# Optimization experiments

Hardware: AMD Instinct MI355X
Metric: run time of the kernel (lower is better)

Reference implementation:

```python
import jax, jax.numpy as jnp
import numpy as np

EMBD_DIM = 768
NUM_HEADS = 12
QKV_DIM = EMBD_DIM // NUM_HEADS  # 64


def setup_inputs() -> dict:
    key = jax.random.key(0)
    k1, k2, k3, k4 = jax.random.split(key, 4)
    B, S = 4, 2048
    X = jax.random.normal(k1, (B, S, EMBD_DIM), dtype=jnp.float32)
    mask = jax.random.randint(k2, (B, S), 0, 2, dtype=jnp.int32)
    scale = 1.0 / np.sqrt(EMBD_DIM)
    W_qkv = jax.random.normal(k3, (EMBD_DIM, 3 * EMBD_DIM), dtype=jnp.float32) * scale
    W_fc = jax.random.normal(k4, (EMBD_DIM, EMBD_DIM), dtype=jnp.float32) * scale
    return {"X": X, "mask": mask, "W_qkv": W_qkv, "W_fc": W_fc}


def reference(X, mask, W_qkv, W_fc):
    B, S, _ = X.shape
    qkv = X @ W_qkv  # (B,S,3*E)
    qkv = qkv.reshape(B, S, NUM_HEADS, 3 * QKV_DIM)
    q, k, v = jnp.split(qkv, 3, axis=-1)  # each (B,S,H,d)
    attn = jnp.einsum('bqhd,bkhd->bhqk', q, k) / np.sqrt(QKV_DIM)
    neg_inf = jnp.finfo(attn.dtype).min
    attn = jnp.where(mask[:, None, None, :] == 0, -jnp.inf, attn)
    attn = jax.nn.softmax(attn, axis=-1)
    out = jnp.einsum('bhqv,bvhd->bqhd', attn, v).reshape(B, S, EMBD_DIM)
    return out @ W_fc
```

## Files before the change

kernel.cpp:

```cpp
#include <hip/hip_runtime.h>
#include <hip/hip_bf16.h>
#include <math.h>

#define NB 4
#define NS 2048
#define NE 768
#define NH 12
#define ND 64
#define NQKV 2304
#define BHN (NB*NH)

typedef __attribute__((ext_vector_type(8))) short bf16x8;
typedef __attribute__((ext_vector_type(4))) float f32x4;
typedef __attribute__((ext_vector_type(16))) float f32x16;
typedef unsigned int uint32;

#define QSCALE (0.125f * 1.44269504f)

__device__ __forceinline__ ushort f2bf(float x){
  __hip_bfloat16 h = __float2bfloat16(x);
  return *reinterpret_cast<ushort*>(&h);
}
__device__ __forceinline__ float bf2f(ushort u){
  __hip_bfloat16 h = *reinterpret_cast<__hip_bfloat16*>(&u);
  return __bfloat162float(h);
}
__device__ __forceinline__ void split2(float x, ushort &hi, ushort &lo){
  ushort h = f2bf(x);
  hi = h;
  lo = f2bf(x - bf2f(h));
}
__device__ __forceinline__ uint32 cvtpk(float lo, float hi){
  uint32 r;
  asm("v_cvt_pk_bf16_f32 %0, %1, %2" : "=v"(r) : "v"(lo), "v"(hi));
  return r;
}
__device__ __forceinline__ void pl32swap(uint32 &a, uint32 &b){
  asm("v_permlane32_swap_b32 %0, %1" : "+v"(a), "+v"(b));
}
__device__ __forceinline__ void gl_lds16(const void* g, void* l){
  __builtin_amdgcn_global_load_lds(
      (const __attribute__((address_space(1))) unsigned int*)g,
      (__attribute__((address_space(3))) unsigned int*)l, 16, 0, 0);
}

__global__ __launch_bounds__(256)
void k_convert_x(const float* __restrict__ X, ushort* __restrict__ H, ushort* __restrict__ L)
{
  const int idx = (blockIdx.x*256 + threadIdx.x)*8;
  float4 x0 = *(const float4*)(X+idx);
  float4 x1 = *(const float4*)(X+idx+4);
  float xs[8] = {x0.x,x0.y,x0.z,x0.w,x1.x,x1.y,x1.z,x1.w};
  bf16x8 vh, vl;
#pragma unroll
  for (int i=0;i<8;++i){
    ushort hi, lo; split2(xs[i], hi, lo);
    vh[i] = (short)hi; vl[i] = (short)lo;
  }
  *(bf16x8*)(H+idx) = vh;
  *(bf16x8*)(L+idx) = vl;
}

__global__ __launch_bounds__(256)
void k_transpose_w(const float* __restrict__ W, ushort* __restrict__ TH, ushort* __restrict__ TL,
                   int K, int N)
{
  __shared__ ushort LH[64][72], LL[64][72];
  const int tid = threadIdx.x;
  const int k0 = blockIdx.y*64, n0 = blockIdx.x*64;
  const int kk = tid >> 4, nn = (tid & 15)*4;
#pragma unroll
  for (int p=0;p<4;++p){
    const int k = kk + p*16;
    float4 v = *(const float4*)(W + (size_t)(k0+k)*N + n0 + nn);
    float xs[4] = {v.x, v.y, v.z, v.w};
#pragma unroll
    for (int c=0;c<4;++c){
      ushort hi, lo; split2(xs[c], hi, lo);
      LH[nn+c][k] = hi; LL[nn+c][k] = lo;
    }
  }
  __syncthreads();
  const int nr = tid >> 2, ch = (tid & 3)*16;
  bf16x8 h0, h1, l0, l1;
#pragma unroll
  for (int i=0;i<8;++i){
    h0[i] = (short)LH[nr][ch+i];   h1[i] = (short)LH[nr][ch+8+i];
    l0[i] = (short)LL[nr][ch+i];   l1[i] = (short)LL[nr][ch+8+i];
  }
  ushort* dh = TH + (size_t)(n0+nr)*K + k0 + ch;
  ushort* dl = TL + (size_t)(n0+nr)*K + k0 + ch;
  *(bf16x8*)dh = h0; *(bf16x8*)(dh+8) = h1;
  *(bf16x8*)dl = l0; *(bf16x8*)(dl+8) = l1;
}

__global__ __launch_bounds__(256)
void k_maskprep(const int* __restrict__ mask, uint32* __restrict__ MW)
{
  const int tid = threadIdx.x;
  const int b = tid >> 6, kt = (tid >> 1) & 31, h = tid & 1;
  uint32 wv = 0;
#pragma unroll
  for (int t=0;t<2;++t){
#pragma unroll
    for (int r=0;r<16;++r){
      const int key = (r&3) + 8*(r>>2) + 4*h + 32*t;
      if (mask[b*NS + kt*64 + key] != 0) wv |= (1u << (r + 16*t));
    }
  }
  MW[tid] = wv;
}

template<int MODE, int NT>
__global__ __launch_bounds__(256)
void k_gemm(const ushort* __restrict__ Ah, const ushort* __restrict__ Al,
            const ushort* __restrict__ Bh, const ushort* __restrict__ Bl,
            float* __restrict__ C,
            ushort* __restrict__ Qo, ushort* __restrict__ Ko, ushort* __restrict__ Vo,
            int M, int N, int K)
{
  __shared__ ushort Ash[4096], Asl[4096], Bsh[4096];
  __shared__ ushort Bsl[NT == 3 ? 4096 : 16];
  const int tid = threadIdx.x;
  const int lane = tid & 63;
  const int w = tid >> 6;
  const int wm = w & 1, wn = w >> 1;
  const int l15 = lane & 15, lg = lane >> 4;
  const int m0 = blockIdx.y*128, n0 = blockIdx.x*128;

  f32x4 acc[4][4] = {};

  const int srow   = tid >> 2;
  const int schunk = tid & 3;
  const int ldst   = tid*8;

  for (int k0 = 0; k0 < K; k0 += 32) {
    if (k0) __syncthreads();
#pragma unroll
    for (int i=0;i<2;++i){
      const int row = i*64 + srow;
      const int kc  = (schunk ^ ((row>>1)&3))*8;
      const size_t ao = (size_t)(m0+row)*K + k0 + kc;
      const size_t bo = (size_t)(n0+row)*K + k0 + kc;
      gl_lds16(Ah+ao, &Ash[i*2048+ldst]);
      gl_lds16(Al+ao, &Asl[i*2048+ldst]);
      gl_lds16(Bh+bo, &Bsh[i*2048+ldst]);
      if (NT == 3) gl_lds16(Bl+bo, &Bsl[i*2048+ldst]);
    }
    __syncthreads();

    bf16x8 fah[4], fal[4], fbh[4], fbl[4];
#pragma unroll
    for (int i=0;i<4;++i){
      const int ra = wm*64 + i*16 + l15;
      const int ca = (lg ^ ((ra>>1)&3))*8;
      fah[i] = *(const bf16x8*)&Ash[ra*32 + ca];
      fal[i] = *(const bf16x8*)&Asl[ra*32 + ca];
      const int rb = wn*64 + i*16 + l15;
      const int cb = (lg ^ ((rb>>1)&3))*8;
      fbh[i] = *(const bf16x8*)&Bsh[rb*32 + cb];
      if (NT == 3) fbl[i] = *(const bf16x8*)&Bsl[rb*32 + cb];
    }
    __builtin_amdgcn_s_setprio(1);
#pragma unroll
    for (int mi=0;mi<4;++mi){
#pragma unroll
      for (int ni=0;ni<4;++ni){
        acc[mi][ni] = __builtin_amdgcn_mfma_f32_16x16x32_bf16(fah[mi], fbh[ni], acc[mi][ni], 0,0,0);
        if (NT == 3)
          acc[mi][ni] = __builtin_amdgcn_mfma_f32_16x16x32_bf16(fah[mi], fbl[ni], acc[mi][ni], 0,0,0);
        acc[mi][ni] = __builtin_amdgcn_mfma_f32_16x16x32_bf16(fal[mi], fbh[ni], acc[mi][ni], 0,0,0);
      }
    }
    __builtin_amdgcn_s_setprio(0);
  }

#pragma unroll
  for (int mi=0;mi<4;++mi){
#pragma unroll
    for (int ni=0;ni<4;++ni){
#pragma unroll
      for (int j=0;j<4;++j){
        const int m = m0 + wm*64 + mi*16 + (lane>>4)*4 + j;
        const int n = n0 + wn*64 + ni*16 + l15;
        const float v = acc[mi][ni][j];
        if (MODE == 0) {
          const int bb = m >> 11, ss = m & 2047;
          const int hh = n / 192, rr = n - hh*192;
          const int d = rr & 63;
          if (rr < 64) {
            Qo[((size_t)(bb*NH + hh)*NS + ss)*ND + d] = f2bf(v * QSCALE);
          } else if (rr < 128) {
            Ko[((size_t)(bb*NH + hh)*NS + ss)*ND + d] = f2bf(v);
          } else {
            Vo[((size_t)(bb*NH + hh)*ND + d)*NS + ss] = f2bf(v);
          }
        } else {
          C[(size_t)m*N + n] = v;
        }
      }
    }
  }
}

__global__ __launch_bounds__(256)
void k_attn(const ushort* __restrict__ Qb, const ushort* __restrict__ Kb,
            const ushort* __restrict__ VTb, const uint32* __restrict__ MW,
            ushort* __restrict__ Ohi, ushort* __restrict__ Olo)
{
  __shared__ ushort Kls[2][4096];
  __shared__ ushort Vls[2][4096];

  const int tid = threadIdx.x;
  const int lane = tid & 63;
  const int w = tid >> 6;
  const int l31 = lane & 31;
  const int h = lane >> 5;
  const int qt = blockIdx.x, head = blockIdx.y, b = blockIdx.z;
  const int bh = b*NH + head;
  const int qglob = qt*128 + w*32 + l31;

  bf16x8 qf[4];
  {
    const ushort* qp = Qb + ((size_t)bh*NS + qglob)*ND + h*8;
#pragma unroll
    for (int s=0;s<4;++s) qf[s] = *(const bf16x8*)(qp + s*16);
  }

  const int srow = (w<<3) + (lane>>3);
  const int scol = ((lane&7) ^ (lane>>3)) << 3;
  const ushort* Kg  = Kb  + (size_t)bh*NS*ND;
  const ushort* VTg = VTb + (size_t)bh*ND*NS;
  const int lbase = (w<<9);

#define STAGE(kt_, bsel_)                                                     \
  {                                                                           \
    _Pragma("unroll")                                                         \
    for (int i_=0;i_<2;++i_){                                                 \
      const int row_ = i_*32 + srow;                                          \
      gl_lds16(Kg  + (size_t)((kt_)*64 + row_)*ND + scol,                     \
               &Kls[bsel_][i_*2048 + lbase]);                                 \
      gl_lds16(VTg + (size_t)row_*NS + (kt_)*64 + scol,                       \
               &Vls[bsel_][i_*2048 + lbase]);                                 \
    }                                                                         \
  }

  f32x16 o0, o1;
#pragma unroll
  for (int r=0;r<16;++r){ o0[r]=0.f; o1[r]=0.f; }
  float m_run = -INFINITY, l_run = 0.f;

  STAGE(0, 0);
  __syncthreads();

  for (int kt = 0; kt < NS/64; ++kt){
    const int buf = kt & 1;
    if (kt + 1 < NS/64) STAGE(kt+1, buf^1);
    const uint32 mw = MW[b*64 + kt*2 + h];

    f32x16 z0, z1;
#pragma unroll
    for (int r=0;r<16;++r){
      const int b0 = ((int)(mw << (31-r))) >> 31;
      const int b1 = ((int)(mw << (15-r))) >> 31;
      z0[r] = __int_as_float(~b0 & 0xFF7FFFFFu);
      z1[r] = __int_as_float(~b1 & 0xFF7FFFFFu);
    }

    const char* kbase = (const char*)&Kls[buf][0];
    __builtin_amdgcn_s_setprio(1);
#pragma unroll
    for (int s=0;s<4;++s){
      const int cb = (s*32 + h*16) ^ ((l31&7)<<4);
      bf16x8 kf0 = *(const bf16x8*)(kbase + l31*128 + cb);
      z0 = __builtin_amdgcn_mfma_f32_32x32x16_bf16(kf0, qf[s], z0, 0,0,0);
      bf16x8 kf1 = *(const bf16x8*)(kbase + (32+l31)*128 + cb);
      z1 = __builtin_amdgcn_mfma_f32_32x32x16_bf16(kf1, qf[s], z1, 0,0,0);
    }
    __builtin_amdgcn_s_setprio(0);

    float tmax = fmaxf(z0[0], z1[0]);
#pragma unroll
    for (int r=1;r<16;++r) tmax = fmaxf(tmax, fmaxf(z0[r], z1[r]));
    tmax = fmaxf(tmax, __shfl_xor(tmax, 32));

    if (!__all(tmax <= m_run)) {
      const float mnew  = fmaxf(m_run, tmax);
      const float msafe = fmaxf(mnew, -1e30f);
      const float alpha = exp2f(m_run - msafe);
      m_run = mnew;
      l_run *= alpha;
#pragma unroll
      for (int r=0;r<16;++r){ o0[r] *= alpha; o1[r] *= alpha; }
    }
    const float mbase = fmaxf(m_run, -1e30f);

    float sc[32];
    float psum = 0.f;
#pragma unroll
    for (int r=0;r<16;++r){
      const float p0 = exp2f(z0[r] - mbase);
      const float p1 = exp2f(z1[r] - mbase);
      sc[r] = p0; sc[16+r] = p1;
      psum += p0 + p1;
    }
    psum += __shfl_xor(psum, 32);
    l_run += psum;

    const char* vbase = (const char*)&Vls[buf][0];
#pragma unroll
    for (int ks=0;ks<4;++ks){
      const int rb = (ks&1)*8 + (ks>>1)*16;
      uint32 d0 = cvtpk(sc[rb+0], sc[rb+1]);
      uint32 d2 = cvtpk(sc[rb+4], sc[rb+5]);
      pl32swap(d0, d2);
      uint32 d1 = cvtpk(sc[rb+2], sc[rb+3]);
      uint32 d3 = cvtpk(sc[rb+6], sc[rb+7]);
      pl32swap(d1, d3);
      union { uint32 u[4]; bf16x8 v; } pf;
      pf.u[0] = d0; pf.u[1] = d1; pf.u[2] = d2; pf.u[3] = d3;
      const int cb = (ks*32 + h*16) ^ ((l31&7)<<4);
      __builtin_amdgcn_s_setprio(1);
      bf16x8 vf0 = *(const bf16x8*)(vbase + l31*128 + cb);
      o0 = __builtin_amdgcn_mfma_f32_32x32x16_bf16(vf0, pf.v, o0, 0,0,0);
      bf16x8 vf1 = *(const bf16x8*)(vbase + (32+l31)*128 + cb);
      o1 = __builtin_amdgcn_mfma_f32_32x32x16_bf16(vf1, pf.v, o1, 0,0,0);
      __builtin_amdgcn_s_setprio(0);
    }
    __syncthreads();
  }

  const float inv = 1.f / l_run;
  const size_t obase = ((size_t)(b*NS + qglob))*NE + head*ND;
#pragma unroll
  for (int a=0;a<2;++a){
#pragma unroll
    for (int rp=0;rp<8;++rp){
      const int r = rp*2;
      const float v0 = (a ? o1[r]   : o0[r])   * inv;
      const float v1 = (a ? o1[r+1] : o0[r+1]) * inv;
      ushort h0,lo0,h1,lo1;
      split2(v0, h0, lo0); split2(v1, h1, lo1);
      const int d = (r&3) + 8*(r>>2) + 4*h + 32*a;
      *(uint32*)(Ohi + obase + d) = (uint32)h0 | ((uint32)h1<<16);
      *(uint32*)(Olo + obase + d) = (uint32)lo0 | ((uint32)lo1<<16);
    }
  }
#undef STAGE
}

extern "C" void kernel_launch(void* const* d_in, const int* in_sizes, int n_in,
                              void* d_out, int out_size, void* d_ws, size_t ws_size,
                              hipStream_t stream)
{
  const float* X    = (const float*)d_in[0];
  const int*   mask = (const int*)d_in[1];
  const float* Wqkv = (const float*)d_in[2];
  const float* Wfc  = (const float*)d_in[3];
  float* out = (float*)d_out;

  char* p = (char*)d_ws;
  const size_t szXE = (size_t)NB*NS*NE;
  const size_t szT  = (size_t)BHN*NS*ND;
  ushort* Xhi = (ushort*)p; p += szXE*2;
  ushort* Xlo = (ushort*)p; p += szXE*2;
  ushort* Wqh = (ushort*)p; p += (size_t)NQKV*NE*2;
  ushort* Wql = (ushort*)p; p += (size_t)NQKV*NE*2;
  ushort* Wfh = (ushort*)p; p += (size_t)NE*NE*2;
  ushort* Wfl = (ushort*)p; p += (size_t)NE*NE*2;
  ushort* Qb  = (ushort*)p; p += szT*2;
  ushort* Kb  = (ushort*)p; p += szT*2;
  ushort* VTb = (ushort*)p; p += szT*2;
  ushort* Ohi = (ushort*)p; p += szXE*2;
  ushort* Olo = (ushort*)p; p += szXE*2;
  uint32* MW  = (uint32*)p; p += 256*4;

  k_convert_x<<<(int)(szXE/2048), 256, 0, stream>>>(X, Xhi, Xlo);
  k_transpose_w<<<dim3(NQKV/64, NE/64), 256, 0, stream>>>(Wqkv, Wqh, Wql, NE, NQKV);
  k_transpose_w<<<dim3(NE/64, NE/64), 256, 0, stream>>>(Wfc, Wfh, Wfl, NE, NE);
  k_maskprep<<<1, 256, 0, stream>>>(mask, MW);
  k_gemm<0,2><<<dim3(NQKV/128, (NB*NS)/128), 256, 0, stream>>>(
      Xhi, Xlo, Wqh, Wql, nullptr, Qb, Kb, VTb, NB*NS, NQKV, NE);
  k_attn<<<dim3(NS/128, NH, NB), 256, 0, stream>>>(Qb, Kb, VTb, MW, Ohi, Olo);
  k_gemm<1,3><<<dim3(NE/128, (NB*NS)/128), 256, 0, stream>>>(
      Ohi, Olo, Wfh, Wfl, out, nullptr, nullptr, nullptr, NB*NS, NE, NE);
}
```

Baseline: 378.6 us.

## Unroll attention loop by two with static buffers and pointer-increment staging

Restructures the flash-attention inner loop to process two key tiles per iteration with compile-time LDS buffer indices. Staging now advances precomputed global pointers instead of recomputing addresses each tile. Masking moves from the MFMA accumulator initial value to a select after the MFMAs, and exp2 switches to the hardware builtin. It also drops the setprio hints and adds a waves-per-EU launch bound. Together these aim to cut scalar and VALU overhead and register pressure, at the risk of extra select work and changed scheduling.

Result: faster. 332.9 us (-12.1%).

```diff
diff --git a/kernel.cpp b/kernel.cpp
--- a/kernel.cpp
+++ b/kernel.cpp
@@ -37,6 +37,13 @@
 }
 __device__ __forceinline__ void pl32swap(uint32 &a, uint32 &b){
   asm("v_permlane32_swap_b32 %0, %1" : "+v"(a), "+v"(b));
+}
+__device__ __forceinline__ float exp2x(float x){
+#if __has_builtin(__builtin_amdgcn_exp2f)
+  return __builtin_amdgcn_exp2f(x);
+#else
+  return exp2f(x);
+#endif
 }
 __device__ __forceinline__ void gl_lds16(const void* g, void* l){
   __builtin_amdgcn_global_load_lds(
@@ -203,7 +210,7 @@
   }
 }
 
-__global__ __launch_bounds__(256)
+__global__ __launch_bounds__(256, 4)
 void k_attn(const ushort* __restrict__ Qb, const ushort* __restrict__ Kb,
             const ushort* __restrict__ VTb, const uint32* __restrict__ MW,
             ushort* __restrict__ Ohi, ushort* __restrict__ Olo)
@@ -216,6 +223,7 @@
   const int w = tid >> 6;
   const int l31 = lane & 31;
   const int h = lane >> 5;
+  const int lx = (l31 & 7) << 4;
   const int qt = blockIdx.x, head = blockIdx.y, b = blockIdx.z;
   const int bh = b*NH + head;
   const int qglob = qt*128 + w*32 + l31;
@@ -229,20 +237,20 @@
 
   const int srow = (w<<3) + (lane>>3);
   const int scol = ((lane&7) ^ (lane>>3)) << 3;
-  const ushort* Kg  = Kb  + (size_t)bh*NS*ND;
-  const ushort* VTg = VTb + (size_t)bh*ND*NS;
+  const ushort* kp0 = Kb  + (size_t)bh*NS*ND + (size_t)srow*ND + scol;
+  const ushort* kp1 = kp0 + 32*ND;
+  const ushort* vp0 = VTb + (size_t)bh*ND*NS + (size_t)srow*NS + scol;
+  const ushort* vp1 = vp0 + (size_t)32*NS;
+  const uint32* mwp = MW + b*64 + h;
   const int lbase = (w<<9);
 
-#define STAGE(kt_, bsel_)                                                     \
+#define STAGE_TO(BUF)                                                         \
   {                                                                           \
-    _Pragma("unroll")                                                         \
-    for (int i_=0;i_<2;++i_){                                                 \
-      const int row_ = i_*32 + srow;                                          \
-      gl_lds16(Kg  + (size_t)((kt_)*64 + row_)*ND + scol,                     \
-               &Kls[bsel_][i_*2048 + lbase]);                                 \
-      gl_lds16(VTg + (size_t)row_*NS + (kt_)*64 + scol,                       \
-               &Vls[bsel_][i_*2048 + lbase]);                                 \
-    }                                                                         \
+    gl_lds16(kp0, &Kls[BUF][lbase]);                                          \
+    gl_lds16(kp1, &Kls[BUF][2048 + lbase]);                                   \
+    gl_lds16(vp0, &Vls[BUF][lbase]);                                          \
+    gl_lds16(vp1, &Vls[BUF][2048 + lbase]);                                   \
+    kp0 += 64*ND; kp1 += 64*ND; vp0 += 64; vp1 += 64;                         \
   }
 
   f32x16 o0, o1;
@@ -250,83 +258,78 @@
   for (int r=0;r<16;++r){ o0[r]=0.f; o1[r]=0.f; }
   float m_run = -INFINITY, l_run = 0.f;
 
-  STAGE(0, 0);
+#define ATTN_TILE(BUF)                                                        \
+  {                                                                           \
+    const uint32 mw = *mwp; mwp += 2;                                         \
+    f32x16 z0, z1;                                                            \
+    _Pragma("unroll")                                                         \
+    for (int r=0;r<16;++r){ z0[r]=0.f; z1[r]=0.f; }                           \
+    const char* kbase = (const char*)&Kls[BUF][0];                            \
+    _Pragma("unroll")                                                         \
+    for (int s=0;s<4;++s){                                                    \
+      const int cb = (s*32 + h*16) ^ lx;                                      \
+      bf16x8 kf0 = *(const bf16x8*)(kbase + l31*128 + cb);                    \
+      z0 = __builtin_amdgcn_mfma_f32_32x32x16_bf16(kf0, qf[s], z0, 0,0,0);    \
+      bf16x8 kf1 = *(const bf16x8*)(kbase + (32+l31)*128 + cb);               \
+      z1 = __builtin_amdgcn_mfma_f32_32x32x16_bf16(kf1, qf[s], z1, 0,0,0);    \
+    }                                                                         \
+    _Pragma("unroll")                                                         \
+    for (int r=0;r<16;++r){                                                   \
+      z0[r] = (mw & (1u<<r))      ? z0[r] : -INFINITY;                        \
+      z1[r] = (mw & (1u<<(16+r))) ? z1[r] : -INFINITY;                        \
+    }                                                                         \
+    float tmax = fmaxf(z0[0], z1[0]);                                         \
+    _Pragma("unroll")                                                         \
+    for (int r=1;r<16;++r) tmax = fmaxf(tmax, fmaxf(z0[r], z1[r]));           \
+    tmax = fmaxf(tmax, __shfl_xor(tmax, 32));                                 \
+    if (!__all(tmax <= m_run)) {                                              \
+      const float mnew  = fmaxf(m_run, tmax);                                 \
+      const float msafe = fmaxf(mnew, -1e30f);                                \
+      const float alpha = exp2x(m_run - msafe);                               \
+      m_run = mnew; l_run *= alpha;                                           \
+      _Pragma("unroll")                                                       \
+      for (int r=0;r<16;++r){ o0[r] *= alpha; o1[r] *= alpha; }               \
+    }                                                                         \
+    const float mbase = fmaxf(m_run, -1e30f);                                 \
+    float psum = 0.f;                                                         \
+    _Pragma("unroll")                                                         \
+    for (int r=0;r<16;++r){                                                   \
+      z0[r] = exp2x(z0[r] - mbase);                                           \
+      z1[r] = exp2x(z1[r] - mbase);                                           \
+      psum += z0[r] + z1[r];                                                  \
+    }                                                                         \
+    psum += __shfl_xor(psum, 32);                                             \
+    l_run += psum;                                                            \
+    const char* vbase = (const char*)&Vls[BUF][0];                            \
+    _Pragma("unroll")                                                         \
+    for (int ks=0;ks<4;++ks){                                                 \
+      const f32x16& zz = (ks < 2) ? z0 : z1;                                  \
+      const int rb = (ks&1)*8;                                                \
+      uint32 d0 = cvtpk(zz[rb+0], zz[rb+1]);                                  \
+      uint32 d2 = cvtpk(zz[rb+4], zz[rb+5]);                                  \
+      pl32swap(d0, d2);                                                       \
+      uint32 d1 = cvtpk(zz[rb+2], zz[rb+3]);                                  \
+      uint32 d3 = cvtpk(zz[rb+6], zz[rb+7]);                                  \
+      pl32swap(d1, d3);                                                       \
+      union { uint32 u[4]; bf16x8 v; } pf;                                    \
+      pf.u[0]=d0; pf.u[1]=d1; pf.u[2]=d2; pf.u[3]=d3;                         \
+      const int cb = (ks*32 + h*16) ^ lx;                                     \
+      bf16x8 vf0 = *(const bf16x8*)(vbase + l31*128 + cb);                    \
+      o0 = __builtin_amdgcn_mfma_f32_32x32x16_bf16(vf0, pf.v, o0, 0,0,0);     \
+      bf16x8 vf1 = *(const bf16x8*)(vbase + (32+l31)*128 + cb);               \
+      o1 = __builtin_amdgcn_mfma_f32_32x32x16_bf16(vf1, pf.v, o1, 0,0,0);     \
+    }                                                                         \
+  }
+
+  STAGE_TO(0);
   __syncthreads();
 
-  for (int kt = 0; kt < NS/64; ++kt){
-    const int buf = kt & 1;
-    if (kt + 1 < NS/64) STAGE(kt+1, buf^1);
-    const uint32 mw = MW[b*64 + kt*2 + h];
-
-    f32x16 z0, z1;
-#pragma unroll
-    for (int r=0;r<16;++r){
-      const int b0 = ((int)(mw << (31-r))) >> 31;
-      const int b1 = ((int)(mw << (15-r))) >> 31;
-      z0[r] = __int_as_float(~b0 & 0xFF7FFFFFu);
-      z1[r] = __int_as_float(~b1 & 0xFF7FFFFFu);
-    }
-
-    const char* kbase = (const char*)&Kls[buf][0];
-    __builtin_amdgcn_s_setprio(1);
-#pragma unroll
-    for (int s=0;s<4;++s){
-      const int cb = (s*32 + h*16) ^ ((l31&7)<<4);
-      bf16x8 kf0 = *(const bf16x8*)(kbase + l31*128 + cb);
-      z0 = __builtin_amdgcn_mfma_f32_32x32x16_bf16(kf0, qf[s], z0, 0,0,0);
-      bf16x8 kf1 = *(const bf16x8*)(kbase + (32+l31)*128 + cb);
-      z1 = __builtin_amdgcn_mfma_f32_32x32x16_bf16(kf1, qf[s], z1, 0,0,0);
-    }
-    __builtin_amdgcn_s_setprio(0);
-
-    float tmax = fmaxf(z0[0], z1[0]);
-#pragma unroll
-    for (int r=1;r<16;++r) tmax = fmaxf(tmax, fmaxf(z0[r], z1[r]));
-    tmax = fmaxf(tmax, __shfl_xor(tmax, 32));
-
-    if (!__all(tmax <= m_run)) {
-      const float mnew  = fmaxf(m_run, tmax);
-      const float msafe = fmaxf(mnew, -1e30f);
-      const float alpha = exp2f(m_run - msafe);
-      m_run = mnew;
-      l_run *= alpha;
-#pragma unroll
-      for (int r=0;r<16;++r){ o0[r] *= alpha; o1[r] *= alpha; }
-    }
-    const float mbase = fmaxf(m_run, -1e30f);
-
-    float sc[32];
-    float psum = 0.f;
-#pragma unroll
-    for (int r=0;r<16;++r){
-      const float p0 = exp2f(z0[r] - mbase);
-      const float p1 = exp2f(z1[r] - mbase);
-      sc[r] = p0; sc[16+r] = p1;
-      psum += p0 + p1;
-    }
-    psum += __shfl_xor(psum, 32);
-    l_run += psum;
-
-    const char* vbase = (const char*)&Vls[buf][0];
-#pragma unroll
-    for (int ks=0;ks<4;++ks){
-      const int rb = (ks&1)*8 + (ks>>1)*16;
-      uint32 d0 = cvtpk(sc[rb+0], sc[rb+1]);
-      uint32 d2 = cvtpk(sc[rb+4], sc[rb+5]);
-      pl32swap(d0, d2);
-      uint32 d1 = cvtpk(sc[rb+2], sc[rb+3]);
-      uint32 d3 = cvtpk(sc[rb+6], sc[rb+7]);
-      pl32swap(d1, d3);
-      union { uint32 u[4]; bf16x8 v; } pf;
-      pf.u[0] = d0; pf.u[1] = d1; pf.u[2] = d2; pf.u[3] = d3;
-      const int cb = (ks*32 + h*16) ^ ((l31&7)<<4);
-      __builtin_amdgcn_s_setprio(1);
-      bf16x8 vf0 = *(const bf16x8*)(vbase + l31*128 + cb);
-      o0 = __builtin_amdgcn_mfma_f32_32x32x16_bf16(vf0, pf.v, o0, 0,0,0);
-      bf16x8 vf1 = *(const bf16x8*)(vbase + (32+l31)*128 + cb);
-      o1 = __builtin_amdgcn_mfma_f32_32x32x16_bf16(vf1, pf.v, o1, 0,0,0);
-      __builtin_amdgcn_s_setprio(0);
-    }
+  for (int kt = 0; kt < NS/64; kt += 2){
+    STAGE_TO(1);
+    ATTN_TILE(0);
+    __syncthreads();
+    if (kt + 2 < NS/64) STAGE_TO(0);
+    ATTN_TILE(1);
     __syncthreads();
   }
 
@@ -346,7 +349,8 @@
       *(uint32*)(Olo + obase + d) = (uint32)lo0 | ((uint32)lo1<<16);
     }
   }
-#undef STAGE
+#undef STAGE_TO
+#undef ATTN_TILE
 }
 
 extern "C" void kernel_launch(void* const* d_in, const int* in_sizes, int n_in,
```
